# Optimization experiments

Measured on AMD Instinct MI355X. Metric: run time of the kernel, lower is better.

## Reference

```python
import jax, jax.numpy as jnp
import numpy as np

B, S, HID, NH = 2, 2048, 2048, 16
HD = HID // NH          # head_size = 128
ROPE_THETA = 10000.0
SCALING = HD ** -0.5


def setup_inputs() -> dict:
    key = jax.random.key(0)
    ks = jax.random.split(key, 8)
    std = 1.0 / np.sqrt(HID)
    inp = {
        "hidden_states": jax.random.normal(ks[0], (B, S, HID), jnp.float32),
        "positions": jnp.broadcast_to(jnp.arange(S, dtype=jnp.int32), (B, S)),
        "wq": jax.random.normal(ks[1], (HID, HID), jnp.float32) * std,
        "bq": jax.random.normal(ks[2], (HID,), jnp.float32) * 0.02,
        "wk": jax.random.normal(ks[3], (HID, HID), jnp.float32) * std,
        "bk": jax.random.normal(ks[4], (HID,), jnp.float32) * 0.02,
        "wv": jax.random.normal(ks[5], (HID, HID), jnp.float32) * std,
        "bv": jax.random.normal(ks[6], (HID,), jnp.float32) * 0.02,
        "wc": jax.random.normal(ks[7], (HID, HID), jnp.float32) * std,
    }
    return inp


def _rope_neox(x, positions):
    # x: [B, S, NH, HD]; positions: [B, S] int
    half = HD // 2
    inv_freq = 1.0 / (ROPE_THETA ** (jnp.arange(half, dtype=jnp.float32) * (2.0 / HD)))
    freqs = positions.astype(jnp.float32)[..., None] * inv_freq      # [B,S,half]
    cos = jnp.cos(freqs)[:, :, None, :]                               # [B,S,1,half]
    sin = jnp.sin(freqs)[:, :, None, :]
    x1, x2 = x[..., :half], x[..., half:]
    return jnp.concatenate([x1 * cos - x2 * sin, x2 * cos + x1 * sin], axis=-1)


def reference(hidden_states, positions, wq, bq, wk, bk, wv, bv, wc):
    # fused QKV projections
    q = hidden_states @ wq + bq
    k = hidden_states @ wk + bk
    v = hidden_states @ wv + bv
    q = q.reshape(B, S, NH, HD)
    k = k.reshape(B, S, NH, HD)
    v = v.reshape(B, S, NH, HD)
    # neox-style rotary embedding over full head dim
    q = _rope_neox(q, positions)
    k = _rope_neox(k, positions)
    # causal self-attention (prefill path of RadixAttention)
    scores = jnp.einsum("bqhd,bkhd->bhqk", q, k) * SCALING
    causal = jnp.tril(jnp.ones((S, S), dtype=bool))
    scores = jnp.where(causal, scores, jnp.finfo(scores.dtype).min)
    probs = jax.nn.softmax(scores, axis=-1)
    attn = jnp.einsum("bhqk,bkhd->bqhd", probs, v).reshape(B, S, HID)
    # output projection (no bias)
    return attn @ wc
```

## Files before the change

kernel.cpp:

```cpp
#include <hip/hip_runtime.h>
#include <stdint.h>

constexpr int Bsz = 2;
constexpr int Ssz = 2048;
constexpr int Hid = 2048;
constexpr int NHd = 16;
constexpr int Hd  = 128;
constexpr int Mrows = Bsz * Ssz;
constexpr float kScale = 0.08838834764831845f;

typedef __bf16 bf16;
typedef __bf16 bf16x8 __attribute__((ext_vector_type(8)));
typedef __bf16 bf16x4 __attribute__((ext_vector_type(4)));
typedef float  f32x4  __attribute__((ext_vector_type(4)));
typedef float  f32x16 __attribute__((ext_vector_type(16)));

__device__ __forceinline__ void gload_lds16(const bf16* g, bf16* l) {
  __builtin_amdgcn_global_load_lds((const __attribute__((address_space(1))) void*)g,
                                   (__attribute__((address_space(3))) void*)l, 16, 0, 0);
}

__device__ __forceinline__ uint32_t pkbf(bf16 a, bf16 b) {
  union { bf16 hh[2]; uint32_t u; } x;
  x.hh[0] = a; x.hh[1] = b;
  return x.u;
}
__device__ __forceinline__ uint32_t pkff(float a, float b) {
  return pkbf((bf16)a, (bf16)b);
}

__global__ void k_cvt(const float* __restrict__ in, bf16* __restrict__ out, int n4) {
  int i = blockIdx.x * blockDim.x + threadIdx.x;
  if (i >= n4) return;
  float4 v = ((const float4*)in)[i];
  bf16x4 o = { (bf16)v.x, (bf16)v.y, (bf16)v.z, (bf16)v.w };
  ((bf16x4*)out)[i] = o;
}

__global__ void k_wtrans(const float* __restrict__ w0, const float* __restrict__ w1,
                         const float* __restrict__ w2, const float* __restrict__ w3,
                         bf16* __restrict__ out) {
  __shared__ float tile[32][33];
  int z = blockIdx.z;
  const float* w = (z == 0) ? w0 : (z == 1) ? w1 : (z == 2) ? w2 : w3;
  bf16* o = out + (size_t)z * Hid * Hid;
  int n0 = blockIdx.x * 32, k0 = blockIdx.y * 32;
  int tx = threadIdx.x, ty = threadIdx.y;
#pragma unroll
  for (int i = 0; i < 4; i++)
    tile[ty + i * 8][tx] = w[(size_t)(k0 + ty + i * 8) * Hid + n0 + tx];
  __syncthreads();
#pragma unroll
  for (int i = 0; i < 4; i++)
    o[(size_t)(n0 + ty + i * 8) * Hid + k0 + tx] = (bf16)tile[tx][ty + i * 8];
}

template <int MODE>
__global__ __launch_bounds__(256, 2) void k_gemm(const bf16* __restrict__ A,
                                                 const bf16* __restrict__ Bt,
                                                 const float* __restrict__ biasq,
                                                 const float* __restrict__ biask,
                                                 const float* __restrict__ biasv,
                                                 bf16* __restrict__ Qo, bf16* __restrict__ Ko,
                                                 bf16* __restrict__ Vo, float* __restrict__ Fo) {
  constexpr int KK = Hid;
  const int z = blockIdx.z;
  const bf16* Bw = Bt + (size_t)z * Hid * Hid;
  const int m0 = blockIdx.y * 128, n0 = blockIdx.x * 128;
  __shared__ bf16 As[128][32];
  __shared__ bf16 Bs[128][32];
  const int tid = threadIdx.x;
  const int lane = tid & 63, wid = tid >> 6;
  const int wr = wid >> 1, wcc = wid & 1;
  const int srow = lane >> 2, scol = (lane & 3) * 8;
  const bf16* Ag = A + (size_t)(m0 + wid * 16 + srow) * KK + scol;
  const bf16* Bg = Bw + (size_t)(n0 + wid * 16 + srow) * KK + scol;
  const int frow = lane & 15, fk8 = (lane >> 4) * 8;
  f32x4 acc[4][4] = {};
  for (int k0 = 0; k0 < KK; k0 += 32) {
    __syncthreads();
    gload_lds16(Ag + k0, &As[wid * 16][0]);
    gload_lds16(Ag + (size_t)64 * KK + k0, &As[64 + wid * 16][0]);
    gload_lds16(Bg + k0, &Bs[wid * 16][0]);
    gload_lds16(Bg + (size_t)64 * KK + k0, &Bs[64 + wid * 16][0]);
    __syncthreads();
    bf16x8 af[4], bfr[4];
#pragma unroll
    for (int i = 0; i < 4; i++) af[i] = *(const bf16x8*)&As[wr * 64 + i * 16 + frow][fk8];
#pragma unroll
    for (int i = 0; i < 4; i++) bfr[i] = *(const bf16x8*)&Bs[wcc * 64 + i * 16 + frow][fk8];
#pragma unroll
    for (int mi = 0; mi < 4; mi++)
#pragma unroll
      for (int ni = 0; ni < 4; ni++)
        acc[mi][ni] = __builtin_amdgcn_mfma_f32_16x16x32_bf16(af[mi], bfr[ni], acc[mi][ni], 0, 0, 0);
  }
  if (MODE == 0) {
    const float* bias = (z == 0) ? biasq : (z == 1) ? biask : biasv;
    bf16* o = (z == 0) ? Qo : (z == 1) ? Ko : Vo;
    const float oscale = (z == 1) ? (float)(0.08838834764831845 * 1.4426950408889634) : 1.0f;
#pragma unroll
    for (int ni = 0; ni < 4; ni++) {
      const int col = n0 + wcc * 64 + ni * 16 + frow;
      const float bb_ = bias[col];
      const int h = col >> 7, hd = col & (Hd - 1);
#pragma unroll
      for (int mi = 0; mi < 4; mi++) {
#pragma unroll
        for (int r = 0; r < 4; r++) {
          const int row = m0 + wr * 64 + mi * 16 + (lane >> 4) * 4 + r;
          const int bb = row >> 11, ss = row & (Ssz - 1);
          o[(((size_t)bb * NHd + h) * Ssz + ss) * Hd + hd] = (bf16)((acc[mi][ni][r] + bb_) * oscale);
        }
      }
    }
  } else {
#pragma unroll
    for (int mi = 0; mi < 4; mi++)
#pragma unroll
      for (int ni = 0; ni < 4; ni++) {
        const int col = n0 + wcc * 64 + ni * 16 + frow;
#pragma unroll
        for (int r = 0; r < 4; r++) {
          const int row = m0 + wr * 64 + mi * 16 + (lane >> 4) * 4 + r;
          Fo[(size_t)row * Hid + col] = acc[mi][ni][r];
        }
      }
  }
}

__global__ void k_rope(bf16* __restrict__ Q, bf16* __restrict__ Kk, const int* __restrict__ pos) {
  const int idx = blockIdx.x * 256 + threadIdx.x;
  const int i = idx & 63;
  const int s = (idx >> 6) & (Ssz - 1);
  const int bh = idx >> 17;
  const int b = bh >> 4;
  const float p = (float)pos[b * Ssz + s];
  const float f = p * exp2f(-(float)i * 0.20762050593046014f);
  float sn, cs;
  sincosf(f, &sn, &cs);
  const size_t base = ((size_t)bh * Ssz + s) * Hd;
  float x1 = (float)Q[base + i], x2 = (float)Q[base + i + 64];
  Q[base + i]      = (bf16)(x1 * cs - x2 * sn);
  Q[base + i + 64] = (bf16)(x2 * cs + x1 * sn);
  x1 = (float)Kk[base + i]; x2 = (float)Kk[base + i + 64];
  Kk[base + i]      = (bf16)(x1 * cs - x2 * sn);
  Kk[base + i + 64] = (bf16)(x2 * cs + x1 * sn);
}

__global__ __launch_bounds__(256, 2) void k_attn(const bf16* __restrict__ Qg,
                                                 const bf16* __restrict__ Kg,
                                                 const bf16* __restrict__ Vg,
                                                 bf16* __restrict__ AO) {
  const int bh = blockIdx.y;
  int qc = blockIdx.x;
  if (bh & 1) qc = 15 - qc;
  const int tid = threadIdx.x, lane = tid & 63, w = tid >> 6;
  const int l31 = lane & 31, h = lane >> 5;
  __shared__ bf16 Ks[64 * 128];
  __shared__ bf16 Vt[128 * 72];
  const size_t hbase = (size_t)bh * Ssz * Hd;
  const int q0 = qc * 128 + w * 32;
  bf16x8 qf[8];
  {
    const bf16* qp = Qg + hbase + (size_t)(q0 + l31) * Hd + h * 8;
#pragma unroll
    for (int c = 0; c < 8; c++) qf[c] = *(const bf16x8*)(qp + c * 16);
  }
  float m = -1e30f, lsum = 0.f;
  f32x16 o[4] = {};
  const int NT = 2 * (qc + 1);
  for (int t = 0; t < NT; ++t) {
    const int kv0 = t * 64;
    __syncthreads();
    {
      const bf16* Kt = Kg + hbase + (size_t)kv0 * Hd;
#pragma unroll
      for (int i = 0; i < 4; i++) {
        const int db  = (w * 4 + i) * 1024 + (lane << 4);
        const int row = db >> 8;
        const int cb  = (db & 255) ^ ((row & 7) << 4);
        gload_lds16(Kt + row * Hd + (cb >> 1), Ks + (w * 4 + i) * 512);
      }
    }
    {
      const int r4  = (tid >> 4) << 2;
      const int hd0 = (tid & 15) << 3;
      bf16x8 vv[4];
#pragma unroll
      for (int p = 0; p < 4; p++)
        vv[p] = *(const bf16x8*)(Vg + hbase + (size_t)(kv0 + r4 + p) * Hd + hd0);
#pragma unroll
      for (int j = 0; j < 8; j++) {
        uint2 wv;
        wv.x = pkbf(vv[0][j], vv[1][j]);
        wv.y = pkbf(vv[2][j], vv[3][j]);
        const int hd = hd0 + j;
        const int cb = (r4 * 2) ^ (((hd >> 3) & 7) << 4);
        *(uint2*)((char*)Vt + hd * 144 + cb) = wv;
      }
    }
    __syncthreads();
    if (kv0 <= q0 + 31) {
      f32x16 s0 = {}, s1 = {};
#pragma unroll
      for (int c = 0; c < 8; c++) {
        const int cb = (c * 32 + h * 16) ^ ((l31 & 7) << 4);
        bf16x8 k0 = *(const bf16x8*)((const char*)Ks + l31 * 256 + cb);
        bf16x8 k1 = *(const bf16x8*)((const char*)Ks + (32 + l31) * 256 + cb);
        s0 = __builtin_amdgcn_mfma_f32_32x32x16_bf16(k0, qf[c], s0, 0, 0, 0);
        s1 = __builtin_amdgcn_mfma_f32_32x32x16_bf16(k1, qf[c], s1, 0, 0, 0);
      }
      if (kv0 + 63 > q0) {
        const int qg = q0 + l31;
        const int kb = kv0 + 4 * h;
#pragma unroll
        for (int r = 0; r < 16; r++) {
          const int cr = (r & 3) + 8 * (r >> 2);
          if (kb + cr > qg)      s0[r] = -1e30f;
          if (kb + 32 + cr > qg) s1[r] = -1e30f;
        }
      }
      float tm = s0[0];
#pragma unroll
      for (int r = 1; r < 16; r++) tm = fmaxf(tm, s0[r]);
#pragma unroll
      for (int r = 0; r < 16; r++) tm = fmaxf(tm, s1[r]);
      tm = fmaxf(tm, __shfl_xor(tm, 32));
      if (!__all(tm - m <= 8.0f)) {
        const float mn = fmaxf(m, tm);
        const float rs = exp2f(m - mn);
        m = mn; lsum *= rs;
#pragma unroll
        for (int ct = 0; ct < 4; ct++)
#pragma unroll
          for (int r = 0; r < 16; r++) o[ct][r] *= rs;
      }
      float ps = 0.f;
#pragma unroll
      for (int r = 0; r < 16; r++) { s0[r] = exp2f(s0[r] - m); ps += s0[r]; }
#pragma unroll
      for (int r = 0; r < 16; r++) { s1[r] = exp2f(s1[r] - m); ps += s1[r]; }
      ps += __shfl_xor(ps, 32);
      lsum += ps;
      uint32_t gw[8][2];
#pragma unroll
      for (int g = 0; g < 4; g++) {
        gw[g][0]     = pkff(s0[4 * g], s0[4 * g + 1]);
        gw[g][1]     = pkff(s0[4 * g + 2], s0[4 * g + 3]);
        gw[4 + g][0] = pkff(s1[4 * g], s1[4 * g + 1]);
        gw[4 + g][1] = pkff(s1[4 * g + 2], s1[4 * g + 3]);
      }
#pragma unroll
      for (int kc = 0; kc < 4; kc++) {
        const uint32_t a0 = gw[2 * kc][0], a1 = gw[2 * kc][1];
        const uint32_t b0 = gw[2 * kc + 1][0], b1 = gw[2 * kc + 1][1];
        const uint32_t sd0 = h ? a0 : b0, sd1 = h ? a1 : b1;
        const uint32_t r0 = (uint32_t)__shfl_xor((int)sd0, 32);
        const uint32_t r1 = (uint32_t)__shfl_xor((int)sd1, 32);
        union { uint32_t u[4]; bf16x8 v; } pa;
        pa.u[0] = h ? r0 : a0; pa.u[1] = h ? r1 : a1;
        pa.u[2] = h ? b0 : r0; pa.u[3] = h ? b1 : r1;
#pragma unroll
        for (int ct = 0; ct < 4; ct++) {
          const int row = ct * 32 + l31;
          const int cb = (kc * 32 + h * 16) ^ (((row >> 3) & 7) << 4);
          bf16x8 vf = *(const bf16x8*)((const char*)Vt + row * 144 + cb);
          o[ct] = __builtin_amdgcn_mfma_f32_32x32x16_bf16(pa.v, vf, o[ct], 0, 0, 0);
        }
      }
    }
  }
  const float linv = 1.0f / lsum;
  float li[16];
#pragma unroll
  for (int r = 0; r < 16; r++)
    li[r] = __shfl(linv, (r & 3) + 8 * (r >> 2) + 4 * h);
  const int b = bh >> 4, hh = bh & 15;
#pragma unroll
  for (int ct = 0; ct < 4; ct++) {
#pragma unroll
    for (int r = 0; r < 16; r++) {
      const int qrow = q0 + (r & 3) + 8 * (r >> 2) + 4 * h;
      AO[((size_t)b * Ssz + qrow) * Hid + hh * Hd + ct * 32 + l31] = (bf16)(o[ct][r] * li[r]);
    }
  }
}

extern "C" void kernel_launch(void* const* d_in, const int* in_sizes, int n_in,
                              void* d_out, int out_size, void* d_ws, size_t ws_size,
                              hipStream_t stream) {
  (void)in_sizes; (void)n_in; (void)out_size; (void)ws_size;
  const float* hidden   = (const float*)d_in[0];
  const int*   positions= (const int*)d_in[1];
  const float* wq = (const float*)d_in[2];
  const float* bq = (const float*)d_in[3];
  const float* wk = (const float*)d_in[4];
  const float* bk = (const float*)d_in[5];
  const float* wv = (const float*)d_in[6];
  const float* bv = (const float*)d_in[7];
  const float* wc = (const float*)d_in[8];
  float* out = (float*)d_out;

  char* ws = (char*)d_ws;
  bf16* WT  = (bf16*)ws;
  bf16* Hbf = (bf16*)(ws + (size_t)4 * Hid * Hid * 2);
  bf16* Qb  = (bf16*)(ws + (size_t)4 * Hid * Hid * 2 + (size_t)Mrows * Hid * 2);
  bf16* Kb  = Qb + (size_t)Mrows * Hid;
  bf16* Vb  = Kb + (size_t)Mrows * Hid;

  k_cvt<<<dim3(Mrows * Hid / 4 / 256), dim3(256), 0, stream>>>(hidden, Hbf, Mrows * Hid / 4);
  k_wtrans<<<dim3(Hid / 32, Hid / 32, 4), dim3(32, 8), 0, stream>>>(wq, wk, wv, wc, WT);
  k_gemm<0><<<dim3(Hid / 128, Mrows / 128, 3), dim3(256), 0, stream>>>(
      Hbf, WT, bq, bk, bv, Qb, Kb, Vb, nullptr);
  k_rope<<<dim3(Bsz * NHd * Ssz * 64 / 256), dim3(256), 0, stream>>>(Qb, Kb, positions);
  k_attn<<<dim3(16, Bsz * NHd), dim3(256), 0, stream>>>(Qb, Kb, Vb, Hbf );
  k_gemm<1><<<dim3(Hid / 128, Mrows / 128, 1), dim3(256), 0, stream>>>(
      Hbf, WT + (size_t)3 * Hid * Hid, nullptr, nullptr, nullptr,
      nullptr, nullptr, nullptr, out);
}
```

Baseline: 317.3 us.

## Rewrite GEMM with 256x128 tiles, double-buffered swizzled LDS and XCD-aware block remap

New measurement: 301.2 us. -5.1%, faster.

```diff
diff --git a/kernel.cpp b/kernel.cpp
--- a/kernel.cpp
+++ b/kernel.cpp
@@ -55,8 +55,28 @@
     o[(size_t)(n0 + ty + i * 8) * Hid + k0 + tx] = (bf16)tile[tx][ty + i * 8];
 }
 
+__device__ __forceinline__ bf16x8 rdfrag(const bf16* t, int row, int kslot) {
+  return *(const bf16x8*)((const char*)t + row * 128 + (((kslot ^ (row & 7)) & 7) << 4));
+}
+
+template <int NB>
+__device__ __forceinline__ void stageN(const bf16* g, bf16* l, int w, int lane) {
+  const int rsub = lane >> 3;
+  const int slot = (lane & 7) ^ rsub;
+#pragma unroll
+  for (int j = 0; j < NB; ++j) {
+    const int blk = w * NB + j;
+    gload_lds16(g + (size_t)(blk * 8 + rsub) * Hid + slot * 8, l + blk * 512);
+  }
+}
+
+#define PH_SYNC()                                      \
+  __builtin_amdgcn_s_barrier();                        \
+  asm volatile("s_waitcnt lgkmcnt(0)" ::: "memory");   \
+  __builtin_amdgcn_sched_barrier(0);
+
 template <int MODE>
-__global__ __launch_bounds__(256, 2) void k_gemm(const bf16* __restrict__ A,
+__global__ __launch_bounds__(512, 2) void k_gemm(const bf16* __restrict__ A,
                                                  const bf16* __restrict__ Bt,
                                                  const float* __restrict__ biasq,
                                                  const float* __restrict__ biask,
@@ -64,51 +84,90 @@
                                                  bf16* __restrict__ Qo, bf16* __restrict__ Ko,
                                                  bf16* __restrict__ Vo, float* __restrict__ Fo) {
   constexpr int KK = Hid;
-  const int z = blockIdx.z;
-  const bf16* Bw = Bt + (size_t)z * Hid * Hid;
-  const int m0 = blockIdx.y * 128, n0 = blockIdx.x * 128;
-  __shared__ bf16 As[128][32];
-  __shared__ bf16 Bs[128][32];
-  const int tid = threadIdx.x;
-  const int lane = tid & 63, wid = tid >> 6;
-  const int wr = wid >> 1, wcc = wid & 1;
-  const int srow = lane >> 2, scol = (lane & 3) * 8;
-  const bf16* Ag = A + (size_t)(m0 + wid * 16 + srow) * KK + scol;
-  const bf16* Bg = Bw + (size_t)(n0 + wid * 16 + srow) * KK + scol;
-  const int frow = lane & 15, fk8 = (lane >> 4) * 8;
+  constexpr int NT = KK / 64;
+  __shared__ bf16 smA[2][256 * 64];
+  __shared__ bf16 smB[2][128 * 64];
+  const int nwg = gridDim.x * gridDim.y;
+  int flat = blockIdx.y * gridDim.x + blockIdx.x;
+  flat = (flat & 7) * (nwg >> 3) + (flat >> 3);
+  const int m0 = (flat / gridDim.x) * 256;
+  const int n0 = (flat % gridDim.x) * 128;
+  const int tid = threadIdx.x, lane = tid & 63, w = tid >> 6;
+  const int wm = w >> 1, wn = w & 1;
+  const int frow = lane & 15, a4 = lane >> 4;
+  const bf16* Ag = A + (size_t)m0 * KK;
+  const bf16* Bg = Bt + (size_t)n0 * KK;
   f32x4 acc[4][4] = {};
-  for (int k0 = 0; k0 < KK; k0 += 32) {
-    __syncthreads();
-    gload_lds16(Ag + k0, &As[wid * 16][0]);
-    gload_lds16(Ag + (size_t)64 * KK + k0, &As[64 + wid * 16][0]);
-    gload_lds16(Bg + k0, &Bs[wid * 16][0]);
-    gload_lds16(Bg + (size_t)64 * KK + k0, &Bs[64 + wid * 16][0]);
-    __syncthreads();
-    bf16x8 af[4], bfr[4];
-#pragma unroll
-    for (int i = 0; i < 4; i++) af[i] = *(const bf16x8*)&As[wr * 64 + i * 16 + frow][fk8];
-#pragma unroll
-    for (int i = 0; i < 4; i++) bfr[i] = *(const bf16x8*)&Bs[wcc * 64 + i * 16 + frow][fk8];
-#pragma unroll
-    for (int mi = 0; mi < 4; mi++)
-#pragma unroll
-      for (int ni = 0; ni < 4; ni++)
-        acc[mi][ni] = __builtin_amdgcn_mfma_f32_16x16x32_bf16(af[mi], bfr[ni], acc[mi][ni], 0, 0, 0);
+  stageN<4>(Ag, smA[0], w, lane);
+  stageN<2>(Bg, smB[0], w, lane);
+  __syncthreads();
+#pragma unroll 2
+  for (int kt = 0; kt < NT; ++kt) {
+    const int cur = kt & 1;
+    const bf16* At = smA[cur];
+    const bf16* Btl = smB[cur];
+    bf16* As2 = smA[cur ^ 1];
+    bf16* Bs2 = smB[cur ^ 1];
+    const int kn = (kt + 1 < NT ? kt + 1 : kt) * 64;
+    bf16x8 af[2][2], bfr[4][2];
+#pragma unroll
+    for (int mi = 0; mi < 2; ++mi)
+#pragma unroll
+      for (int kk = 0; kk < 2; ++kk)
+        af[mi][kk] = rdfrag(At, wm * 64 + mi * 16 + frow, kk * 4 + a4);
+#pragma unroll
+    for (int ni = 0; ni < 4; ++ni)
+#pragma unroll
+      for (int kk = 0; kk < 2; ++kk)
+        bfr[ni][kk] = rdfrag(Btl, wn * 64 + ni * 16 + frow, kk * 4 + a4);
+    stageN<4>(Ag + kn, As2, w, lane);
+    PH_SYNC();
+    __builtin_amdgcn_s_setprio(1);
+#pragma unroll
+    for (int mi = 0; mi < 2; ++mi)
+#pragma unroll
+      for (int ni = 0; ni < 4; ++ni)
+#pragma unroll
+        for (int kk = 0; kk < 2; ++kk)
+          acc[mi][ni] = __builtin_amdgcn_mfma_f32_16x16x32_bf16(
+              af[mi][kk], bfr[ni][kk], acc[mi][ni], 0, 0, 0);
+    __builtin_amdgcn_s_setprio(0);
+    __builtin_amdgcn_s_barrier();
+#pragma unroll
+    for (int mi = 0; mi < 2; ++mi)
+#pragma unroll
+      for (int kk = 0; kk < 2; ++kk)
+        af[mi][kk] = rdfrag(At, wm * 64 + (2 + mi) * 16 + frow, kk * 4 + a4);
+    stageN<2>(Bg + kn, Bs2, w, lane);
+    PH_SYNC();
+    __builtin_amdgcn_s_setprio(1);
+#pragma unroll
+    for (int mi = 0; mi < 2; ++mi)
+#pragma unroll
+      for (int ni = 0; ni < 4; ++ni)
+#pragma unroll
+        for (int kk = 0; kk < 2; ++kk)
+          acc[2 + mi][ni] = __builtin_amdgcn_mfma_f32_16x16x32_bf16(
+              af[mi][kk], bfr[ni][kk], acc[2 + mi][ni], 0, 0, 0);
+    __builtin_amdgcn_s_setprio(0);
+    asm volatile("s_waitcnt vmcnt(0)" ::: "memory");
+    __builtin_amdgcn_s_barrier();
   }
   if (MODE == 0) {
+    const int z = n0 >> 11;
     const float* bias = (z == 0) ? biasq : (z == 1) ? biask : biasv;
     bf16* o = (z == 0) ? Qo : (z == 1) ? Ko : Vo;
     const float oscale = (z == 1) ? (float)(0.08838834764831845 * 1.4426950408889634) : 1.0f;
 #pragma unroll
-    for (int ni = 0; ni < 4; ni++) {
-      const int col = n0 + wcc * 64 + ni * 16 + frow;
-      const float bb_ = bias[col];
-      const int h = col >> 7, hd = col & (Hd - 1);
-#pragma unroll
-      for (int mi = 0; mi < 4; mi++) {
-#pragma unroll
-        for (int r = 0; r < 4; r++) {
-          const int row = m0 + wr * 64 + mi * 16 + (lane >> 4) * 4 + r;
+    for (int ni = 0; ni < 4; ++ni) {
+      const int col = n0 + wn * 64 + ni * 16 + frow;
+      const float bb_ = bias[col & 2047];
+      const int h = (col >> 7) & 15, hd = col & (Hd - 1);
+#pragma unroll
+      for (int mi = 0; mi < 4; ++mi) {
+#pragma unroll
+        for (int r = 0; r < 4; ++r) {
+          const int row = m0 + wm * 64 + mi * 16 + a4 * 4 + r;
           const int bb = row >> 11, ss = row & (Ssz - 1);
           o[(((size_t)bb * NHd + h) * Ssz + ss) * Hd + hd] = (bf16)((acc[mi][ni][r] + bb_) * oscale);
         }
@@ -116,13 +175,13 @@
     }
   } else {
 #pragma unroll
-    for (int mi = 0; mi < 4; mi++)
-#pragma unroll
-      for (int ni = 0; ni < 4; ni++) {
-        const int col = n0 + wcc * 64 + ni * 16 + frow;
-#pragma unroll
-        for (int r = 0; r < 4; r++) {
-          const int row = m0 + wr * 64 + mi * 16 + (lane >> 4) * 4 + r;
+    for (int mi = 0; mi < 4; ++mi)
+#pragma unroll
+      for (int ni = 0; ni < 4; ++ni) {
+        const int col = n0 + wn * 64 + ni * 16 + frow;
+#pragma unroll
+        for (int r = 0; r < 4; ++r) {
+          const int row = m0 + wm * 64 + mi * 16 + a4 * 4 + r;
           Fo[(size_t)row * Hid + col] = acc[mi][ni][r];
         }
       }
@@ -311,11 +370,11 @@
 
   k_cvt<<<dim3(Mrows * Hid / 4 / 256), dim3(256), 0, stream>>>(hidden, Hbf, Mrows * Hid / 4);
   k_wtrans<<<dim3(Hid / 32, Hid / 32, 4), dim3(32, 8), 0, stream>>>(wq, wk, wv, wc, WT);
-  k_gemm<0><<<dim3(Hid / 128, Mrows / 128, 3), dim3(256), 0, stream>>>(
+  k_gemm<0><<<dim3(48, 16), dim3(512), 0, stream>>>(
       Hbf, WT, bq, bk, bv, Qb, Kb, Vb, nullptr);
   k_rope<<<dim3(Bsz * NHd * Ssz * 64 / 256), dim3(256), 0, stream>>>(Qb, Kb, positions);
   k_attn<<<dim3(16, Bsz * NHd), dim3(256), 0, stream>>>(Qb, Kb, Vb, Hbf );
-  k_gemm<1><<<dim3(Hid / 128, Mrows / 128, 1), dim3(256), 0, stream>>>(
+  k_gemm<1><<<dim3(16, 16), dim3(512), 0, stream>>>(
       Hbf, WT + (size_t)3 * Hid * Hid, nullptr, nullptr, nullptr,
       nullptr, nullptr, nullptr, out);
 }
```
